# Kernel tuning notes

Measured on AMD Instinct MI355X. Metric: run time of the kernel, lower is better.

Reference implementation:

```python
import jax, jax.numpy as jnp
import numpy as np
from jax import lax

NEG = -1e30  # log-space 'zero' that stays finite for stable grads


def _logadd3(a, b, c):
    m = jnp.maximum(jnp.maximum(a, b), c)
    return m + jnp.log(jnp.exp(a - m) + jnp.exp(b - m) + jnp.exp(c - m))


def _logadd2(a, b):
    m = jnp.maximum(a, b)
    return m + jnp.log(jnp.exp(a - m) + jnp.exp(b - m))


def setup_inputs() -> dict:
    key = jax.random.key(0)
    k1, k2, k3 = jax.random.split(key, 3)
    B, T, V, L = 64, 2000, 512, 200
    logits = jax.random.normal(k1, (B, T, V), dtype=jnp.float32)
    # keep input lengths well above 2*L+1 so all paths are feasible
    input_lengths = (T - jax.random.randint(k2, (B,), 0, 256)).astype(jnp.int32)
    targets = jax.random.randint(k3, (B, L), 0, V, dtype=jnp.int32)  # 0 == pad == blank
    return {"logits": logits, "input_lengths": input_lengths, "targets": targets}


def ctc_loss_sum(logits, input_lengths, targets):
    B, T, V = logits.shape
    L = targets.shape[1]
    S = 2 * L + 1

    lp = jax.nn.log_softmax(logits, axis=-1)  # [B,T,V]

    # compact nonzero targets per row (masked_select equivalent, fixed shape)
    mask = targets != 0
    tlen = mask.sum(-1)  # [B] target_lengths
    pos = jnp.where(mask, jnp.cumsum(mask, axis=1) - 1, L)
    compact = jnp.zeros_like(targets).at[jnp.arange(B)[:, None], pos].set(targets, mode="drop")

    # extended label sequence: blank, y1, blank, y2, ..., blank  -> [B,S]
    s_idx = jnp.arange(S)
    lab_idx = jnp.clip((s_idx - 1) // 2, 0, L - 1)
    ext = jnp.where(s_idx % 2 == 1, compact[:, lab_idx], 0)  # [B,S]

    # skip transition s-2 -> s allowed iff label at s is non-blank and differs from s-2
    ext_m2 = jnp.pad(ext, ((0, 0), (2, 0)))[:, :S]
    skip_ok = (ext != 0) & (ext != ext_m2) & (s_idx >= 2)  # [B,S]

    lpT = jnp.transpose(lp, (1, 0, 2))  # [T,B,V], scan over time

    # init: alpha_0[0]=lp(blank), alpha_0[1]=lp(y1)
    lp0_ext = jnp.take_along_axis(lpT[0], ext[:, :2], axis=1)  # [B,2]
    alpha0 = jnp.full((B, S), NEG, dtype=lp.dtype).at[:, :2].set(lp0_ext)

    def step(alpha, inp):
        lp_t, t = inp
        a1 = jnp.pad(alpha, ((0, 0), (1, 0)), constant_values=NEG)[:, :S]
        a2 = jnp.pad(alpha, ((0, 0), (2, 0)), constant_values=NEG)[:, :S]
        a2 = jnp.where(skip_ok, a2, NEG)
        lp_e = jnp.take_along_axis(lp_t, ext, axis=1)  # [B,S]
        new = _logadd3(alpha, a1, a2) + lp_e
        active = (t < input_lengths)[:, None]
        return jnp.where(active, new, alpha), None

    alphaT, _ = lax.scan(step, alpha0, (lpT[1:], jnp.arange(1, T)))

    # read out at final blank (2*tlen) and final label (2*tlen-1)
    e1 = (2 * tlen)[:, None]
    e2 = (2 * tlen - 1)
    a1 = jnp.take_along_axis(alphaT, e1, axis=1)[:, 0]
    a2 = jnp.where(e2 >= 0,
                   jnp.take_along_axis(alphaT, jnp.clip(e2, 0)[:, None], axis=1)[:, 0],
                   NEG)
    ll = _logadd2(a1, a2)  # [B] log p(targets | logits)
    return -jnp.sum(ll)


def reference(logits, input_lengths, targets):
    return ctc_loss_sum(logits, input_lengths, targets)
```

## Files before the change

kernel.cpp:

```cpp
#include <hip/hip_runtime.h>

#define B_ 64
#define T_ 2000
#define V_ 512
#define L_ 200
#define CPR 7


__device__ __forceinline__ float dpp_shr1_f(float x) {
  return __int_as_float(__builtin_amdgcn_update_dpp(0, __float_as_int(x), 0x138, 0xf, 0xf, true));
}
__device__ __forceinline__ int dpp_shr1_i(int x) {
  return __builtin_amdgcn_update_dpp(0, x, 0x138, 0xf, 0xf, true);
}
#define DPPADD(v, ctrl, rmask)                                                              \
  v += __int_as_float(__builtin_amdgcn_update_dpp(0, __float_as_int(v), ctrl, rmask, 0xf, true));

__global__ void kz(float* __restrict__ out) { out[0] = 0.0f; }

__global__ __launch_bounds__(512, 1) void ctc_fused(const float* __restrict__ logits,
                                                    const int* __restrict__ lens,
                                                    const int* __restrict__ targets,
                                                    float* __restrict__ out) {
  const int b = blockIdx.x;
  const int wid = threadIdx.x >> 6;
  const int lane = threadIdx.x & 63;

  __shared__ __align__(16) float ring[2][CPR][8][256];
  __shared__ __align__(16) float ringbl[2][CPR][8];
  __shared__ __align__(16) float scr[CPR][2][512];
  __shared__ int cmp[256];
  __shared__ int tl_s;
  __shared__ float sval[512];
  __shared__ int sE[64];

  if (wid == 0) {
    cmp[lane] = 0; cmp[64 + lane] = 0; cmp[128 + lane] = 0; cmp[192 + lane] = 0;
    int base = 0;
#pragma unroll
    for (int cc = 0; cc < 4; ++cc) {
      const int l = cc * 64 + lane;
      const int v = (l < L_) ? targets[b * L_ + l] : 0;
      const unsigned long long mk = __ballot(v != 0);
      const int pos = base + __popcll(mk & ((1ull << lane) - 1ull));
      if (v != 0) cmp[pos] = v;
      base += __popcll(mk);
    }
    if (lane == 0) tl_s = base;
  }
  __syncthreads();

  const int len = lens[b];
  const int nfull = len >> 3;
  const int rem = len & 7;
  const int nch = nfull + (rem ? 1 : 0);
  const int R = (nch + CPR - 1) / CPR;
  const int4 c4 = *(const int4*)(&cmp[4 * lane]);

  const int l0 = 4 * lane;
  const bool v0 = l0 + 0 < L_, v1 = l0 + 1 < L_, v2 = l0 + 2 < L_, v3 = l0 + 3 < L_;

  float a0 = 0.f, a1 = 0.f, a2 = 0.f, a3 = 0.f, a4 = 0.f, a5 = 0.f, a6 = 0.f, a7 = 0.f;
  int E = 0;
  float fac = 1.0f;
  float m0 = 0.f, m1 = 0.f, m2 = 0.f, m3 = 0.f;
  float4 LQ0[8], LQ1[8];
  float4 BLa0, BLb0, BLa1, BLb1;

  if (wid == CPR) {
    const int cm1 = __shfl_up(c4.w, 1);
    m0 = (lane > 0 && c4.x != 0 && c4.x != cm1) ? 1.0f : 0.0f;
    m1 = (c4.y != 0 && c4.y != c4.x) ? 1.0f : 0.0f;
    m2 = (c4.z != 0 && c4.z != c4.y) ? 1.0f : 0.0f;
    m3 = (c4.w != 0 && c4.w != c4.z) ? 1.0f : 0.0f;
    if (lane == 0) a0 = 1.0f;
    __builtin_amdgcn_s_setprio(1);
  }

  auto produce = [&](int rp) {
    const int c = rp * CPR + wid;
    if (c >= nch) return;
    const int buf = rp & 1;
    const float* rowp = logits + (size_t)b * (T_ * V_) + (size_t)c * (8 * V_);
    float4 X[16];
#pragma unroll
    for (int r = 0; r < 8; ++r) {
      X[2 * r] = *(const float4*)(rowp + r * V_ + 4 * lane);
      X[2 * r + 1] = *(const float4*)(rowp + r * V_ + 256 + 4 * lane);
    }
#pragma unroll
    for (int r = 0; r < 8; ++r) {
      const float4 xe = X[2 * r], xo = X[2 * r + 1];
      const float e0 = __expf(xe.x), e1 = __expf(xe.y), e2 = __expf(xe.z), e3 = __expf(xe.w);
      const float e4 = __expf(xo.x), e5 = __expf(xo.y), e6 = __expf(xo.z), e7 = __expf(xo.w);
      float s = ((e0 + e1) + (e2 + e3)) + ((e4 + e5) + (e6 + e7));
      DPPADD(s, 0x111, 0xf); DPPADD(s, 0x112, 0xf); DPPADD(s, 0x114, 0xf);
      DPPADD(s, 0x118, 0xf); DPPADD(s, 0x142, 0xa); DPPADD(s, 0x143, 0xc);
      const float sum = __int_as_float(__builtin_amdgcn_readlane(__float_as_int(s), 63));
      const float inv = 32.0f / sum;
      float* sc = &scr[wid][r & 1][0];
      *(float4*)(sc + 4 * lane) = make_float4(e0, e1, e2, e3);
      *(float4*)(sc + 256 + 4 * lane) = make_float4(e4, e5, e6, e7);
      asm volatile("s_waitcnt lgkmcnt(0)" ::: "memory");
      float4 h;
      h.x = v0 ? sc[c4.x] * inv : 0.0f;
      h.y = v1 ? sc[c4.y] * inv : 0.0f;
      h.z = v2 ? sc[c4.z] * inv : 0.0f;
      h.w = v3 ? sc[c4.w] * inv : 0.0f;
      *(float4*)(&ring[buf][wid][r][4 * lane]) = h;
      if (lane == 0) ringbl[buf][wid][r] = e0 * inv;
    }
  };

#define LDCHUNK(S, BUF, K)                                                   \
  {                                                                          \
    const int bf_ = (BUF), kk_ = (K);                                        \
    _Pragma("unroll") for (int u = 0; u < 8; ++u)                            \
        LQ##S[u] = *(const float4*)(&ring[bf_][kk_][u][4 * lane]);           \
    BLa##S = *(const float4*)(&ringbl[bf_][kk_][0]);                         \
    BLb##S = *(const float4*)(&ringbl[bf_][kk_][4]);                         \
  }

#define STEP8(S, CIDX, MASKED)                                               \
  {                                                                          \
    const int tf_ = (CIDX) * 8;                                              \
    const float blv_[8] = {BLa##S.x, BLa##S.y, BLa##S.z, BLa##S.w,           \
                           BLb##S.x, BLb##S.y, BLb##S.z, BLb##S.w};          \
    _Pragma("unroll") for (int u = 0; u < 8; ++u) {                          \
      const float4 hq = LQ##S[u];                                            \
      const float qx = hq.x, qy = hq.y, qz = hq.z, qw = hq.w;                \
      const float pbv = blv_[u];                                             \
      const float s1 = dpp_shr1_f(a7) * fac;                 \
      float n0 = (a0 + s1) * pbv;                                            \
      float n1 = fmaf(m0, s1, a0 + a1) * qx;                                 \
      float n2 = (a2 + a1) * pbv;                                            \
      float n3 = fmaf(m1, a1, a2 + a3) * qy;                                 \
      float n4 = (a4 + a3) * pbv;                                            \
      float n5 = fmaf(m2, a3, a4 + a5) * qz;                                 \
      float n6 = (a6 + a5) * pbv;                                            \
      float n7 = fmaf(m3, a5, a6 + a7) * qw;                                 \
      if (MASKED) {                                                          \
        const bool act = (tf_ + u) < len;                                    \
        n0 = act ? n0 : a0; n1 = act ? n1 : a1;                              \
        n2 = act ? n2 : a2; n3 = act ? n3 : a3;                              \
        n4 = act ? n4 : a4; n5 = act ? n5 : a5;                              \
        n6 = act ? n6 : a6; n7 = act ? n7 : a7;                              \
      }                                                                      \
      a0 = n0; a1 = n1; a2 = n2; a3 = n3;                                    \
      a4 = n4; a5 = n5; a6 = n6; a7 = n7;                                    \
    }                                                                        \
  }

#define RENORM                                                               \
  {                                                                          \
    const float mx = fmaxf(fmaxf(fmaxf(a0, a1), fmaxf(a2, a3)),              \
                           fmaxf(fmaxf(a4, a5), fmaxf(a6, a7)));             \
    const bool dead = (mx == 0.0f);                                          \
    int e_ = (int)((__float_as_uint(mx) >> 23) & 0xff) - 127;                \
    if (dead) e_ = 0;                                                        \
    const float sc_ = __int_as_float((unsigned)(127 - e_) << 23);            \
    a0 *= sc_; a1 *= sc_; a2 *= sc_; a3 *= sc_;                              \
    a4 *= sc_; a5 *= sc_; a6 *= sc_; a7 *= sc_;                              \
    const int En_ = E + e_;                                                  \
    const int EnP_ = dpp_shr1_i(En_);                                        \
    E = dead ? EnP_ : En_;                                                   \
    const int Ep_ = dpp_shr1_i(E);                                           \
    const int d_ = Ep_ - E;                                                  \
    int dc_ = d_ < -126 ? -126 : (d_ > 126 ? 126 : d_);                      \
    fac = (d_ < -126) ? 0.0f : __int_as_float((unsigned)(dc_ + 127) << 23);  \
  }

  if (wid < CPR) produce(0);
  __syncthreads();

  for (int r = 0; r < R; ++r) {
    if (wid < CPR) {
      if (r + 1 < R) produce(r + 1);
    } else {
      const int c0 = r * CPR;
      int kn = nfull - c0;
      if (kn > CPR) kn = CPR;
      if (kn > 0) {
        LDCHUNK(0, r & 1, 0);
        for (int k = 0; k < kn; ++k) {
          if (k & 1) {
            if (k + 1 < kn) LDCHUNK(0, r & 1, k + 1);
            STEP8(1, 0, 0);
          } else {
            if (k + 1 < kn) LDCHUNK(1, r & 1, k + 1);
            STEP8(0, 0, 0);
          }
          RENORM;
        }
      }
    }
    __syncthreads();
  }

  if (wid == CPR) {
    if (rem) {
      const int cM = nfull;
      const int rM = cM / CPR;
      const int kM = cM - rM * CPR;
      LDCHUNK(0, rM & 1, kM);
      STEP8(0, cM, 1);
    }
    sval[lane * 8 + 0] = a0; sval[lane * 8 + 1] = a1;
    sval[lane * 8 + 2] = a2; sval[lane * 8 + 3] = a3;
    sval[lane * 8 + 4] = a4; sval[lane * 8 + 5] = a5;
    sval[lane * 8 + 6] = a6; sval[lane * 8 + 7] = a7;
    sE[lane] = E;
    asm volatile("s_waitcnt lgkmcnt(0)" ::: "memory");
    if (lane == 0) {
      const int tl = tl_s;
      const int e1 = 2 * tl;
      const int e2 = e1 - 1;
      const float v1r = sval[e1];
      const int E1 = sE[e1 >> 3];
      const float v2r = (e2 >= 0) ? sval[e2] : 0.0f;
      const int E2 = (e2 >= 0) ? sE[e2 >> 3] : E1;
      const int Em = (E1 > E2) ? E1 : E2;
      const float v = ldexpf(v1r, E1 - Em) + ldexpf(v2r, E2 - Em);
      const float ll = __logf(v) + (float)Em * 0.69314718056f - (float)len * 3.46573590280f;
      atomicAdd(out, -ll);
    }
  }
#undef LDCHUNK
#undef STEP8
#undef RENORM
}

extern "C" void kernel_launch(void* const* d_in, const int* in_sizes, int n_in,
                              void* d_out, int out_size, void* d_ws, size_t ws_size,
                              hipStream_t stream) {
  const float* logits = (const float*)d_in[0];
  const int* input_lengths = (const int*)d_in[1];
  const int* targets = (const int*)d_in[2];
  float* out = (float*)d_out;
  (void)d_ws; (void)ws_size; (void)in_sizes; (void)n_in; (void)out_size;

  kz<<<1, 1, 0, stream>>>(out);
  ctc_fused<<<B_, 512, 0, stream>>>(logits, input_lengths, targets, out);
}
```

Measured before the change: 467.0 us.

## Split CTC recursion into forward and backward halves meeting in the middle

Each batch row now runs in two blocks. One runs the alpha recursion forward over the first half of the time chunks, the other runs a beta recursion backward from the end over the remaining chunks. A new small combine kernel takes the dot product of the forward alphas and the one-step-propagated betas, with exponent bookkeeping, to produce the log-likelihood. This halves the serial dependency chain per block and doubles the grid from 64 to 128 blocks, so more of the GPU is used, at the cost of an extra kernel launch, a workspace round trip, and more complex backward-transition code.

```diff
diff --git a/kernel.cpp b/kernel.cpp
--- a/kernel.cpp
+++ b/kernel.cpp
@@ -13,6 +13,12 @@
 __device__ __forceinline__ int dpp_shr1_i(int x) {
   return __builtin_amdgcn_update_dpp(0, x, 0x138, 0xf, 0xf, true);
 }
+__device__ __forceinline__ float dpp_shl1_f(float x) {
+  return __int_as_float(__builtin_amdgcn_update_dpp(0, __float_as_int(x), 0x130, 0xf, 0xf, true));
+}
+__device__ __forceinline__ int dpp_shl1_i(int x) {
+  return __builtin_amdgcn_update_dpp(0, x, 0x130, 0xf, 0xf, true);
+}
 #define DPPADD(v, ctrl, rmask)                                                              \
   v += __int_as_float(__builtin_amdgcn_update_dpp(0, __float_as_int(v), ctrl, rmask, 0xf, true));
 
@@ -21,8 +27,13 @@
 __global__ __launch_bounds__(512, 1) void ctc_fused(const float* __restrict__ logits,
                                                     const int* __restrict__ lens,
                                                     const int* __restrict__ targets,
-                                                    float* __restrict__ out) {
-  const int b = blockIdx.x;
+                                                    float* __restrict__ AF,
+                                                    int* __restrict__ EF,
+                                                    float* __restrict__ DD,
+                                                    int* __restrict__ EB) {
+  const int bx = blockIdx.x;
+  const int b = bx >> 1;
+  const int dirb = bx & 1;
   const int wid = threadIdx.x >> 6;
   const int lane = threadIdx.x & 63;
 
@@ -31,8 +42,6 @@
   __shared__ __align__(16) float scr[CPR][2][512];
   __shared__ int cmp[256];
   __shared__ int tl_s;
-  __shared__ float sval[512];
-  __shared__ int sE[64];
 
   if (wid == 0) {
     cmp[lane] = 0; cmp[64 + lane] = 0; cmp[128 + lane] = 0; cmp[192 + lane] = 0;
@@ -54,7 +63,9 @@
   const int nfull = len >> 3;
   const int rem = len & 7;
   const int nch = nfull + (rem ? 1 : 0);
-  const int R = (nch + CPR - 1) / CPR;
+  const int Cf = nch >> 1;
+  const int Ntot = dirb ? (nch - Cf) : Cf;
+  const int R = (Ntot + CPR - 1) / CPR;
   const int4 c4 = *(const int4*)(&cmp[4 * lane]);
 
   const int l0 = 4 * lane;
@@ -63,7 +74,7 @@
   float a0 = 0.f, a1 = 0.f, a2 = 0.f, a3 = 0.f, a4 = 0.f, a5 = 0.f, a6 = 0.f, a7 = 0.f;
   int E = 0;
   float fac = 1.0f;
-  float m0 = 0.f, m1 = 0.f, m2 = 0.f, m3 = 0.f;
+  float m0 = 0.f, m1 = 0.f, m2 = 0.f, m3 = 0.f, m0n = 0.f;
   float4 LQ0[8], LQ1[8];
   float4 BLa0, BLb0, BLa1, BLb1;
 
@@ -73,14 +84,23 @@
     m1 = (c4.y != 0 && c4.y != c4.x) ? 1.0f : 0.0f;
     m2 = (c4.z != 0 && c4.z != c4.y) ? 1.0f : 0.0f;
     m3 = (c4.w != 0 && c4.w != c4.z) ? 1.0f : 0.0f;
-    if (lane == 0) a0 = 1.0f;
+    m0n = dpp_shl1_f(m0);
+    if (!dirb) {
+      if (lane == 0) a0 = 1.0f;
+    } else {
+      const int st = 2 * tl_s;
+      if (lane == (st >> 3)) {
+        const int e = st & 7;
+        a0 = (e == 0) ? 1.0f : 0.0f; a1 = (e == 1) ? 1.0f : 0.0f;
+        a2 = (e == 2) ? 1.0f : 0.0f; a3 = (e == 3) ? 1.0f : 0.0f;
+        a4 = (e == 4) ? 1.0f : 0.0f; a5 = (e == 5) ? 1.0f : 0.0f;
+        a6 = (e == 6) ? 1.0f : 0.0f; a7 = (e == 7) ? 1.0f : 0.0f;
+      }
+    }
     __builtin_amdgcn_s_setprio(1);
   }
 
-  auto produce = [&](int rp) {
-    const int c = rp * CPR + wid;
-    if (c >= nch) return;
-    const int buf = rp & 1;
+  auto produce = [&](int c, int buf) {
     const float* rowp = logits + (size_t)b * (T_ * V_) + (size_t)c * (8 * V_);
     float4 X[16];
 #pragma unroll
@@ -121,38 +141,52 @@
     BLb##S = *(const float4*)(&ringbl[bf_][kk_][4]);                         \
   }
 
-#define STEP8(S, CIDX, MASKED)                                               \
-  {                                                                          \
-    const int tf_ = (CIDX) * 8;                                              \
+#define STEP8F(S)                                                            \
+  {                                                                          \
     const float blv_[8] = {BLa##S.x, BLa##S.y, BLa##S.z, BLa##S.w,           \
                            BLb##S.x, BLb##S.y, BLb##S.z, BLb##S.w};          \
     _Pragma("unroll") for (int u = 0; u < 8; ++u) {                          \
       const float4 hq = LQ##S[u];                                            \
-      const float qx = hq.x, qy = hq.y, qz = hq.z, qw = hq.w;                \
       const float pbv = blv_[u];                                             \
       const float s1 = dpp_shr1_f(a7) * fac;                 \
       float n0 = (a0 + s1) * pbv;                                            \
-      float n1 = fmaf(m0, s1, a0 + a1) * qx;                                 \
+      float n1 = fmaf(m0, s1, a0 + a1) * hq.x;                               \
       float n2 = (a2 + a1) * pbv;                                            \
-      float n3 = fmaf(m1, a1, a2 + a3) * qy;                                 \
+      float n3 = fmaf(m1, a1, a2 + a3) * hq.y;                               \
       float n4 = (a4 + a3) * pbv;                                            \
-      float n5 = fmaf(m2, a3, a4 + a5) * qz;                                 \
+      float n5 = fmaf(m2, a3, a4 + a5) * hq.z;                               \
       float n6 = (a6 + a5) * pbv;                                            \
-      float n7 = fmaf(m3, a5, a6 + a7) * qw;                                 \
-      if (MASKED) {                                                          \
-        const bool act = (tf_ + u) < len;                                    \
-        n0 = act ? n0 : a0; n1 = act ? n1 : a1;                              \
-        n2 = act ? n2 : a2; n3 = act ? n3 : a3;                              \
-        n4 = act ? n4 : a4; n5 = act ? n5 : a5;                              \
-        n6 = act ? n6 : a6; n7 = act ? n7 : a7;                              \
-      }                                                                      \
+      float n7 = fmaf(m3, a5, a6 + a7) * hq.w;                               \
       a0 = n0; a1 = n1; a2 = n2; a3 = n3;                                    \
       a4 = n4; a5 = n5; a6 = n6; a7 = n7;                                    \
     }                                                                        \
   }
 
-#define RENORM                                                               \
-  {                                                                          \
+#define STEP8B(S, UHI)                                                       \
+  {                                                                          \
+    const float blv_[8] = {BLa##S.x, BLa##S.y, BLa##S.z, BLa##S.w,           \
+                           BLb##S.x, BLb##S.y, BLb##S.z, BLb##S.w};          \
+    _Pragma("unroll") for (int u = 7; u >= 0; --u) {                         \
+      if (u <= (UHI)) {                                                      \
+        const float4 hq = LQ##S[u];                                          \
+        const float pbv = blv_[u];                                           \
+        const float sa = dpp_shl1_f(a0) * fac;              \
+        const float sb = dpp_shl1_f(a1) * fac;                               \
+        float n0 = (a0 + a1) * pbv;                                          \
+        float n1 = fmaf(m1, a3, a1 + a2) * hq.x;                             \
+        float n2 = (a2 + a3) * pbv;                                          \
+        float n3 = fmaf(m2, a5, a3 + a4) * hq.y;                             \
+        float n4 = (a4 + a5) * pbv;                                          \
+        float n5 = fmaf(m3, a7, a5 + a6) * hq.z;                             \
+        float n6 = (a6 + a7) * pbv;                                          \
+        float n7 = fmaf(m0n, sb, a7 + sa) * hq.w;                            \
+        a0 = n0; a1 = n1; a2 = n2; a3 = n3;                                  \
+        a4 = n4; a5 = n5; a6 = n6; a7 = n7;                                  \
+      }                                                                      \
+    }                                                                        \
+  }
+
+#define RENORM_COMMON                                                        \
     const float mx = fmaxf(fmaxf(fmaxf(a0, a1), fmaxf(a2, a3)),              \
                            fmaxf(fmaxf(a4, a5), fmaxf(a6, a7)));             \
     const bool dead = (mx == 0.0f);                                          \
@@ -161,7 +195,11 @@
     const float sc_ = __int_as_float((unsigned)(127 - e_) << 23);            \
     a0 *= sc_; a1 *= sc_; a2 *= sc_; a3 *= sc_;                              \
     a4 *= sc_; a5 *= sc_; a6 *= sc_; a7 *= sc_;                              \
-    const int En_ = E + e_;                                                  \
+    const int En_ = E + e_;
+
+#define RENORMF                                                              \
+  {                                                                          \
+    RENORM_COMMON                                                            \
     const int EnP_ = dpp_shr1_i(En_);                                        \
     E = dead ? EnP_ : En_;                                                   \
     const int Ep_ = dpp_shr1_i(E);                                           \
@@ -170,27 +208,53 @@
     fac = (d_ < -126) ? 0.0f : __int_as_float((unsigned)(dc_ + 127) << 23);  \
   }
 
-  if (wid < CPR) produce(0);
+#define RENORMB                                                              \
+  {                                                                          \
+    RENORM_COMMON                                                            \
+    const int EnP_ = dpp_shl1_i(En_);                                        \
+    E = dead ? EnP_ : En_;                                                   \
+    const int Ep_ = dpp_shl1_i(E);                                           \
+    const int d_ = Ep_ - E;                                                  \
+    int dc_ = d_ < -126 ? -126 : (d_ > 126 ? 126 : d_);                      \
+    fac = (d_ < -126) ? 0.0f : __int_as_float((unsigned)(dc_ + 127) << 23);  \
+  }
+
+  if (wid < CPR) {
+    const int j = wid;
+    if (j < Ntot) produce(dirb ? (nch - 1 - j) : j, 0);
+  }
   __syncthreads();
 
   for (int r = 0; r < R; ++r) {
     if (wid < CPR) {
-      if (r + 1 < R) produce(r + 1);
+      const int j = (r + 1) * CPR + wid;
+      if (r + 1 < R && j < Ntot) produce(dirb ? (nch - 1 - j) : j, (r + 1) & 1);
     } else {
-      const int c0 = r * CPR;
-      int kn = nfull - c0;
+      int kn = Ntot - r * CPR;
       if (kn > CPR) kn = CPR;
-      if (kn > 0) {
-        LDCHUNK(0, r & 1, 0);
+      LDCHUNK(0, r & 1, 0);
+      if (!dirb) {
         for (int k = 0; k < kn; ++k) {
           if (k & 1) {
             if (k + 1 < kn) LDCHUNK(0, r & 1, k + 1);
-            STEP8(1, 0, 0);
+            STEP8F(1);
           } else {
             if (k + 1 < kn) LDCHUNK(1, r & 1, k + 1);
-            STEP8(0, 0, 0);
+            STEP8F(0);
           }
-          RENORM;
+          RENORMF;
+        }
+      } else {
+        for (int k = 0; k < kn; ++k) {
+          const int uh = (r == 0 && k == 0 && rem) ? (rem - 1) : 7;
+          if (k & 1) {
+            if (k + 1 < kn) LDCHUNK(0, r & 1, k + 1);
+            STEP8B(1, uh);
+          } else {
+            if (k + 1 < kn) LDCHUNK(1, r & 1, k + 1);
+            STEP8B(0, uh);
+          }
+          RENORMB;
         }
       }
     }
@@ -198,36 +262,63 @@
   }
 
   if (wid == CPR) {
-    if (rem) {
-      const int cM = nfull;
-      const int rM = cM / CPR;
-      const int kM = cM - rM * CPR;
-      LDCHUNK(0, rM & 1, kM);
-      STEP8(0, cM, 1);
-    }
-    sval[lane * 8 + 0] = a0; sval[lane * 8 + 1] = a1;
-    sval[lane * 8 + 2] = a2; sval[lane * 8 + 3] = a3;
-    sval[lane * 8 + 4] = a4; sval[lane * 8 + 5] = a5;
-    sval[lane * 8 + 6] = a6; sval[lane * 8 + 7] = a7;
-    sE[lane] = E;
-    asm volatile("s_waitcnt lgkmcnt(0)" ::: "memory");
-    if (lane == 0) {
-      const int tl = tl_s;
-      const int e1 = 2 * tl;
-      const int e2 = e1 - 1;
-      const float v1r = sval[e1];
-      const int E1 = sE[e1 >> 3];
-      const float v2r = (e2 >= 0) ? sval[e2] : 0.0f;
-      const int E2 = (e2 >= 0) ? sE[e2 >> 3] : E1;
-      const int Em = (E1 > E2) ? E1 : E2;
-      const float v = ldexpf(v1r, E1 - Em) + ldexpf(v2r, E2 - Em);
-      const float ll = __logf(v) + (float)Em * 0.69314718056f - (float)len * 3.46573590280f;
-      atomicAdd(out, -ll);
+    if (!dirb) {
+      *(float4*)(AF + b * 512 + lane * 8) = make_float4(a0, a1, a2, a3);
+      *(float4*)(AF + b * 512 + lane * 8 + 4) = make_float4(a4, a5, a6, a7);
+      EF[b * 64 + lane] = E;
+    } else {
+      const float sa = dpp_shl1_f(a0) * fac;
+      const float sb = dpp_shl1_f(a1) * fac;
+      const float d0 = a0 + a1;
+      const float d1 = fmaf(m1, a3, a1 + a2);
+      const float d2 = a2 + a3;
+      const float d3 = fmaf(m2, a5, a3 + a4);
+      const float d4 = a4 + a5;
+      const float d5 = fmaf(m3, a7, a5 + a6);
+      const float d6 = a6 + a7;
+      const float d7 = fmaf(m0n, sb, a7 + sa);
+      *(float4*)(DD + b * 512 + lane * 8) = make_float4(d0, d1, d2, d3);
+      *(float4*)(DD + b * 512 + lane * 8 + 4) = make_float4(d4, d5, d6, d7);
+      EB[b * 64 + lane] = E;
     }
   }
 #undef LDCHUNK
-#undef STEP8
-#undef RENORM
+#undef STEP8F
+#undef STEP8B
+#undef RENORM_COMMON
+#undef RENORMF
+#undef RENORMB
+}
+
+__global__ __launch_bounds__(64) void kcomb(const int* __restrict__ lens,
+                                            const float* __restrict__ AF,
+                                            const int* __restrict__ EF,
+                                            const float* __restrict__ DD,
+                                            const int* __restrict__ EB,
+                                            float* __restrict__ out) {
+  const int b = blockIdx.x;
+  const int lane = threadIdx.x;
+  const float4 f0 = *(const float4*)(AF + b * 512 + lane * 8);
+  const float4 f1 = *(const float4*)(AF + b * 512 + lane * 8 + 4);
+  const float4 g0 = *(const float4*)(DD + b * 512 + lane * 8);
+  const float4 g1 = *(const float4*)(DD + b * 512 + lane * 8 + 4);
+  const float dot = ((f0.x * g0.x + f0.y * g0.y) + (f0.z * g0.z + f0.w * g0.w)) +
+                    ((f1.x * g1.x + f1.y * g1.y) + (f1.z * g1.z + f1.w * g1.w));
+  const int Es = EF[b * 64 + lane] + EB[b * 64 + lane];
+  const bool z = (dot == 0.0f);
+  int Ek = z ? (-(1 << 28)) : Es;
+#pragma unroll
+  for (int off = 32; off; off >>= 1) {
+    const int o = __shfl_xor(Ek, off);
+    Ek = o > Ek ? o : Ek;
+  }
+  float v = z ? 0.0f : ldexpf(dot, Es - Ek);
+#pragma unroll
+  for (int off = 32; off; off >>= 1) v += __shfl_xor(v, off);
+  if (lane == 0) {
+    const float ll = __logf(v) + (float)Ek * 0.69314718056f - (float)lens[b] * 3.46573590280f;
+    atomicAdd(out, -ll);
+  }
 }
 
 extern "C" void kernel_launch(void* const* d_in, const int* in_sizes, int n_in,
@@ -237,8 +328,13 @@
   const int* input_lengths = (const int*)d_in[1];
   const int* targets = (const int*)d_in[2];
   float* out = (float*)d_out;
-  (void)d_ws; (void)ws_size; (void)in_sizes; (void)n_in; (void)out_size;
+  float* AF = (float*)d_ws;
+  int* EF = (int*)(AF + B_ * 512);
+  float* DD = (float*)(EF + B_ * 64);
+  int* EB = (int*)(DD + B_ * 512);
+  (void)in_sizes; (void)n_in; (void)out_size; (void)ws_size;
 
   kz<<<1, 1, 0, stream>>>(out);
-  ctc_fused<<<B_, 512, 0, stream>>>(logits, input_lengths, targets, out);
-}
+  ctc_fused<<<2 * B_, 512, 0, stream>>>(logits, input_lengths, targets, AF, EF, DD, EB);
+  kcomb<<<B_, 64, 0, stream>>>(input_lengths, AF, EF, DD, EB, out);
+}
```

Result: faster. 396.1 us (-15.2%).
